# Kernel tuning notes

Hardware: AMD Instinct MI355X
Metric: run time of the kernel (lower is better)

The kernel has to match this reference:

```python
import jax, jax.numpy as jnp
import numpy as np

D_MODEL = 1024
D_FF = 2048
N_EXPERTS = 8
Z_LOSS_COEF = 0.001


def setup_inputs() -> dict:
    key = jax.random.key(0)
    kx, kr, k1, k3, k2 = jax.random.split(key, 5)
    s_in = 1.0 / np.sqrt(D_MODEL)
    s_ff = 1.0 / np.sqrt(D_FF)
    return {
        "x": jax.random.normal(kx, (4, 2048, D_MODEL), dtype=jnp.float32),
        # router: nn.Linear(d_model, num_experts, bias=False) -> weight [E, D]
        "Wr": jax.random.normal(kr, (N_EXPERTS, D_MODEL), dtype=jnp.float32) * s_in,
        # stacked expert weights, torch Linear layout [out, in]
        "W1": jax.random.normal(k1, (N_EXPERTS, D_FF, D_MODEL), dtype=jnp.float32) * s_in,
        "W3": jax.random.normal(k3, (N_EXPERTS, D_FF, D_MODEL), dtype=jnp.float32) * s_in,
        "W2": jax.random.normal(k2, (N_EXPERTS, D_MODEL, D_FF), dtype=jnp.float32) * s_ff,
    }


def reference(x, Wr, W1, W3, W2):
    B, S, D = x.shape
    E = Wr.shape[0]
    xf = x.reshape(B * S, D)          # [T, D]
    T = xf.shape[0]

    # --- router ---
    logits = xf @ Wr.T                # [T, E]
    probs = jax.nn.softmax(logits, axis=-1)
    top2_p, top2_i = jax.lax.top_k(probs, 2)          # [T, 2]
    top2_p = top2_p / (jnp.sum(top2_p, axis=-1, keepdims=True) + 1e-9)

    # dense gate matrix: zero for unselected experts (same math as index_add combine)
    gates = jnp.zeros((T, E), jnp.float32).at[jnp.arange(T)[:, None], top2_i].add(top2_p)

    # --- experts (SwiGLU), computed per-expert over all tokens, masked by gates ---
    h1 = jax.nn.silu(jnp.einsum('td,efd->etf', xf, W1))   # [E, T, F]
    h3 = jnp.einsum('td,efd->etf', xf, W3)                 # [E, T, F]
    y = jnp.einsum('etf,edf->etd', h1 * h3, W2)            # [E, T, D]
    out = jnp.einsum('etd,te->td', y.astype(jnp.float32), gates)
    out = out.astype(x.dtype).reshape(B, S, D)

    # --- losses ---
    z = jax.nn.logsumexp(logits.astype(jnp.float32), axis=-1)
    router_loss = Z_LOSS_COEF * jnp.mean(z * z)

    importance = jnp.sum(probs.astype(jnp.float32), axis=0) / T   # [E]
    top1 = top2_i[:, 0]
    load = jnp.zeros((E,), jnp.float32).at[top1].add(1.0) / T
    aux_loss = jnp.sum(importance * load) * E

    return out, router_loss, aux_loss
```

## Files before the change

kernel.cpp:

```cpp
#include <hip/hip_runtime.h>
#include <stdint.h>

#define NT 8192
#define DM 1024
#define DF 2048
#define RT_BLOCKS 256

typedef __attribute__((ext_vector_type(8))) short short8;
typedef __attribute__((ext_vector_type(4))) float f32x4;

__device__ __forceinline__ unsigned short f2bf(float f) {
  uint32_t x = __float_as_uint(f);
  return (unsigned short)((x + 0x7fffu + ((x >> 16) & 1u)) >> 16);
}

__device__ __forceinline__ void gload16(const void* g, void* l) {
  __builtin_amdgcn_global_load_lds(
      (const __attribute__((address_space(1))) uint32_t*)g,
      (__attribute__((address_space(3))) uint32_t*)l, 16, 0, 0);
}

__global__ void k_cvtw(const float4* __restrict__ w1, const float4* __restrict__ w3,
                       const float4* __restrict__ w2,
                       ushort4* __restrict__ w13, ushort4* __restrict__ w2bf) {
  int s = blockIdx.y;
  const float4* src = (s == 0) ? w1 : (s == 1) ? w3 : w2;
  int n4 = 8 * DF * DM / 4;
  int i = blockIdx.x * blockDim.x + threadIdx.x;
  int st = gridDim.x * blockDim.x;
  for (; i < n4; i += st) {
    float4 v = src[i];
    ushort4 o;
    o.x = f2bf(v.x); o.y = f2bf(v.y); o.z = f2bf(v.z); o.w = f2bf(v.w);
    if (s == 2) {
      w2bf[i] = o;
    } else {
      int e = i >> 19;
      int rem = i & ((1 << 19) - 1);
      int f = rem >> 8;
      int k4 = rem & 255;
      w13[((size_t)e << 20) + (size_t)(2 * f + s) * 256 + k4] = o;
    }
  }
}

__global__ void k_router(const float* __restrict__ x, const float* __restrict__ wr,
                         int* cntb, int* cnt1, float* imp, float* z2,
                         int* epack, float2* gts, unsigned short* __restrict__ xbf) {
  int lane = threadIdx.x & 63;
  int wid = threadIdx.x >> 6;
  const float4* w4 = (const float4*)wr;

  float imp_acc[8] = {0.f, 0.f, 0.f, 0.f, 0.f, 0.f, 0.f, 0.f};
  float z2_acc = 0.f;
  int cb_acc[8] = {0, 0, 0, 0, 0, 0, 0, 0};
  int c1_acc[8] = {0, 0, 0, 0, 0, 0, 0, 0};

  for (int t = blockIdx.x * 4 + wid; t < NT; t += RT_BLOCKS * 4) {
    const float4* x4 = (const float4*)(x + (size_t)t * DM);
    ushort4* xb4 = (ushort4*)(xbf + (size_t)t * DM);
    float4 xv[4];
    #pragma unroll
    for (int j = 0; j < 4; ++j) {
      xv[j] = x4[lane + 64 * j];
      ushort4 o;
      o.x = f2bf(xv[j].x); o.y = f2bf(xv[j].y); o.z = f2bf(xv[j].z); o.w = f2bf(xv[j].w);
      xb4[lane + 64 * j] = o;
    }
    float p[8];
    #pragma unroll
    for (int e = 0; e < 8; ++e) p[e] = 0.f;
    #pragma unroll
    for (int j = 0; j < 4; ++j) {
      #pragma unroll
      for (int e = 0; e < 8; ++e) {
        float4 wv = w4[e * 256 + lane + 64 * j];
        p[e] += xv[j].x * wv.x + xv[j].y * wv.y + xv[j].z * wv.z + xv[j].w * wv.w;
      }
    }
    #pragma unroll
    for (int off = 32; off > 0; off >>= 1) {
      #pragma unroll
      for (int e = 0; e < 8; ++e) p[e] += __shfl_down(p[e], off);
    }
    if (lane == 0) {
      float m = p[0];
      #pragma unroll
      for (int e = 1; e < 8; ++e) m = fmaxf(m, p[e]);
      float pr[8], s = 0.f;
      #pragma unroll
      for (int e = 0; e < 8; ++e) { pr[e] = expf(p[e] - m); s += pr[e]; }
      float inv = 1.f / s;
      #pragma unroll
      for (int e = 0; e < 8; ++e) pr[e] *= inv;
      float z = m + logf(s);
      int e0 = 0; float b0 = p[0];
      #pragma unroll
      for (int e = 1; e < 8; ++e) { if (p[e] > b0) { b0 = p[e]; e0 = e; } }
      int e1 = -1; float b1 = -1e30f;
      #pragma unroll
      for (int e = 0; e < 8; ++e) { if (e != e0 && p[e] > b1) { b1 = p[e]; e1 = e; } }
      float p0 = 0.f, p1 = 0.f;
      #pragma unroll
      for (int e = 0; e < 8; ++e) {
        p0 = (e == e0) ? pr[e] : p0;
        p1 = (e == e1) ? pr[e] : p1;
      }
      float gs = p0 + p1 + 1e-9f;
      epack[t] = e0 | (e1 << 16);
      gts[t] = make_float2(p0 / gs, p1 / gs);
      z2_acc += z * z;
      #pragma unroll
      for (int e = 0; e < 8; ++e) {
        imp_acc[e] += pr[e];
        cb_acc[e] += (e == e0) + (e == e1);
        c1_acc[e] += (e == e0);
      }
    }
  }

  __shared__ float simp[4][8];
  __shared__ float sz2[4];
  __shared__ int scb[4][8];
  __shared__ int sc1[4][8];
  if (lane == 0) {
    #pragma unroll
    for (int e = 0; e < 8; ++e) { simp[wid][e] = imp_acc[e]; scb[wid][e] = cb_acc[e]; sc1[wid][e] = c1_acc[e]; }
    sz2[wid] = z2_acc;
  }
  __syncthreads();
  int tid = threadIdx.x;
  if (tid < 8) {
    float s = simp[0][tid] + simp[1][tid] + simp[2][tid] + simp[3][tid];
    int b = scb[0][tid] + scb[1][tid] + scb[2][tid] + scb[3][tid];
    int o = sc1[0][tid] + sc1[1][tid] + sc1[2][tid] + sc1[3][tid];
    atomicAdd(&imp[tid], s);
    atomicAdd(&cntb[tid], b);
    atomicAdd(&cnt1[tid], o);
  } else if (tid == 8) {
    atomicAdd(z2, sz2[0] + sz2[1] + sz2[2] + sz2[3]);
  }
}

__global__ void k_finalize(const int* cntb, const int* cnt1, const float* imp,
                           const float* z2, int* offs, float* otail) {
  if (threadIdx.x == 0 && blockIdx.x == 0) {
    int o = 0;
    for (int e = 0; e < 8; ++e) { offs[e] = o; o += cntb[e]; }
    otail[0] = 1e-3f * z2[0] / (float)NT;
    float aux = 0.f;
    for (int e = 0; e < 8; ++e)
      aux += (imp[e] / (float)NT) * ((float)cnt1[e] / (float)NT);
    otail[1] = aux * 8.f;
  }
}

__global__ void k_scatter(const int* __restrict__ epack, const float2* __restrict__ gts,
                          const int* __restrict__ offs,
                          int* __restrict__ btok, int* __restrict__ pos) {
  int e = blockIdx.x;
  int lane = threadIdx.x;
  int base = offs[e];
  int run = 0;
  for (int j0 = 0; j0 < 2 * NT; j0 += 64) {
    int j = j0 + lane;
    int t = j >> 1;
    int ep = epack[t];
    int sel = (j & 1) ? (ep >> 16) : (ep & 0xffff);
    bool f = (sel == e);
    unsigned long long m = __ballot(f);
    int rank = __popcll(m & ((1ull << lane) - 1ull));
    if (f) {
      int slot = base + run + rank;
      btok[slot] = t;
      pos[j] = slot;
    }
    run += __popcll(m);
  }
}

__global__ __launch_bounds__(512, 2) void k_ffn1(
    const unsigned short* __restrict__ xb,
    const unsigned short* __restrict__ w13,
    const int* __restrict__ offs, const int* __restrict__ cnts,
    const int* __restrict__ btok,
    unsigned short* __restrict__ hg) {
  int e = blockIdx.z;
  int cnt = cnts[e];
  int m0 = blockIdx.y * 256;
  if (m0 >= cnt) return;
  int n0 = blockIdx.x * 256;
  int off = offs[e];
  __shared__ __align__(16) short As[2][256 * 64];
  __shared__ __align__(16) short Bs[2][256 * 64];
  __shared__ int tok[256];
  int tid = threadIdx.x, lane = tid & 63, wid = tid >> 6;
  if (tid < 256) {
    int r = m0 + tid; if (r > cnt - 1) r = cnt - 1;
    tok[tid] = btok[off + r];
  }
  __syncthreads();

  int rin = lane >> 3;
  int scol = (((lane & 7) ^ rin)) * 8;
  const unsigned short* w13e = w13 + ((size_t)e << 22);
  const unsigned short* asrc[4];
  const unsigned short* bsrc[4];
  int dofs[4];
  #pragma unroll
  for (int i = 0; i < 4; ++i) {
    int ch = wid * 4 + i;
    int rr = ch * 8 + rin;
    asrc[i] = xb + (size_t)tok[rr] * DM + scol;
    bsrc[i] = w13e + (size_t)(n0 + rr) * DM + scol;
    dofs[i] = ch * 512;
  }

  int wm = wid >> 2, wn = wid & 3;
  int g = lane >> 4;
  int l7 = lane & 7;
  int fr = lane & 15;
  f32x4 acc[8][4] = {};

  #pragma unroll
  for (int i = 0; i < 4; ++i) {
    gload16(asrc[i], &As[0][dofs[i]]);
    gload16(bsrc[i], &Bs[0][dofs[i]]);
  }
  __syncthreads();

  int cur = 0;
  const int NK = DM / 64;
  for (int kt = 0; kt < NK; ++kt) {
    if (kt + 1 < NK) {
      int k0 = (kt + 1) * 64;
      #pragma unroll
      for (int i = 0; i < 4; ++i) {
        gload16(asrc[i] + k0, &As[cur ^ 1][dofs[i]]);
        gload16(bsrc[i] + k0, &Bs[cur ^ 1][dofs[i]]);
      }
    }
    #pragma unroll
    for (int kk = 0; kk < 2; ++kk) {
      int G = kk * 4 + g;
      short8 a[8], b[4];
      #pragma unroll
      for (int mi = 0; mi < 8; ++mi) {
        int r = wm * 128 + mi * 16 + fr;
        a[mi] = *(const short8*)&As[cur][r * 64 + ((G ^ l7) * 8)];
      }
      #pragma unroll
      for (int ni = 0; ni < 4; ++ni) {
        int r = wn * 64 + ni * 16 + fr;
        b[ni] = *(const short8*)&Bs[cur][r * 64 + ((G ^ l7) * 8)];
      }
      #pragma unroll
      for (int mi = 0; mi < 8; ++mi) {
        #pragma unroll
        for (int ni = 0; ni < 4; ++ni)
          acc[mi][ni] = __builtin_amdgcn_mfma_f32_16x16x32_bf16(a[mi], b[ni], acc[mi][ni], 0, 0, 0);
      }
    }
    __syncthreads();
    cur ^= 1;
  }

  int c = lane & 15, r4 = (lane >> 4) * 4;
  bool evenc = ((c & 1) == 0);
  #pragma unroll
  for (int mi = 0; mi < 8; ++mi) {
    #pragma unroll
    for (int rg = 0; rg < 4; ++rg) {
      int gr = m0 + wm * 128 + mi * 16 + r4 + rg;
      #pragma unroll
      for (int ni = 0; ni < 4; ++ni) {
        float a1 = acc[mi][ni][rg];
        float a3 = __shfl_xor(a1, 1);
        if (evenc && gr < cnt) {
          int f = (n0 + wn * 64 + ni * 16 + c) >> 1;
          float h = (a1 / (1.f + __expf(-a1))) * a3;
          hg[(size_t)(off + gr) * DF + f] = f2bf(h);
        }
      }
    }
  }
}

__global__ __launch_bounds__(512, 2) void k_ffn2(
    const unsigned short* __restrict__ hg,
    const unsigned short* __restrict__ w2b,
    const int* __restrict__ offs, const int* __restrict__ cnts,
    float* __restrict__ ys) {
  int e = blockIdx.z;
  int cnt = cnts[e];
  int m0 = blockIdx.y * 256;
  if (m0 >= cnt) return;
  int n0 = blockIdx.x * 256;
  int off = offs[e];
  __shared__ __align__(16) short As[2][256 * 64];
  __shared__ __align__(16) short Bs[2][256 * 64];
  int tid = threadIdx.x, lane = tid & 63, wid = tid >> 6;

  int rin = lane >> 3;
  int scol = (((lane & 7) ^ rin)) * 8;
  const unsigned short* w2e = w2b + ((size_t)e << 21);
  const unsigned short* asrc[4];
  const unsigned short* bsrc[4];
  int dofs[4];
  #pragma unroll
  for (int i = 0; i < 4; ++i) {
    int ch = wid * 4 + i;
    int rr = ch * 8 + rin;
    int ar = m0 + rr; if (ar > cnt - 1) ar = cnt - 1;
    asrc[i] = hg + (size_t)(off + ar) * DF + scol;
    bsrc[i] = w2e + (size_t)(n0 + rr) * DF + scol;
    dofs[i] = ch * 512;
  }

  int wm = wid >> 2, wn = wid & 3;
  int g = lane >> 4;
  int l7 = lane & 7;
  int fr = lane & 15;
  f32x4 acc[8][4] = {};

  #pragma unroll
  for (int i = 0; i < 4; ++i) {
    gload16(asrc[i], &As[0][dofs[i]]);
    gload16(bsrc[i], &Bs[0][dofs[i]]);
  }
  __syncthreads();

  int cur = 0;
  const int NK = DF / 64;
  for (int kt = 0; kt < NK; ++kt) {
    if (kt + 1 < NK) {
      int k0 = (kt + 1) * 64;
      #pragma unroll
      for (int i = 0; i < 4; ++i) {
        gload16(asrc[i] + k0, &As[cur ^ 1][dofs[i]]);
        gload16(bsrc[i] + k0, &Bs[cur ^ 1][dofs[i]]);
      }
    }
    #pragma unroll
    for (int kk = 0; kk < 2; ++kk) {
      int G = kk * 4 + g;
      short8 a[8], b[4];
      #pragma unroll
      for (int mi = 0; mi < 8; ++mi) {
        int r = wm * 128 + mi * 16 + fr;
        a[mi] = *(const short8*)&As[cur][r * 64 + ((G ^ l7) * 8)];
      }
      #pragma unroll
      for (int ni = 0; ni < 4; ++ni) {
        int r = wn * 64 + ni * 16 + fr;
        b[ni] = *(const short8*)&Bs[cur][r * 64 + ((G ^ l7) * 8)];
      }
      #pragma unroll
      for (int mi = 0; mi < 8; ++mi) {
        #pragma unroll
        for (int ni = 0; ni < 4; ++ni)
          acc[mi][ni] = __builtin_amdgcn_mfma_f32_16x16x32_bf16(a[mi], b[ni], acc[mi][ni], 0, 0, 0);
      }
    }
    __syncthreads();
    cur ^= 1;
  }

  int c = lane & 15, r4 = (lane >> 4) * 4;
  #pragma unroll
  for (int mi = 0; mi < 8; ++mi) {
    #pragma unroll
    for (int rg = 0; rg < 4; ++rg) {
      int gr = m0 + wm * 128 + mi * 16 + r4 + rg;
      if (gr < cnt) {
        float* yrow = ys + (size_t)(off + gr) * DM + n0;
        #pragma unroll
        for (int ni = 0; ni < 4; ++ni)
          yrow[wn * 64 + ni * 16 + c] = acc[mi][ni][rg];
      }
    }
  }
}

__global__ void k_gather(const float* __restrict__ ys, const int* __restrict__ pos,
                         const float2* __restrict__ gts, float* __restrict__ out) {
  int idx = blockIdx.x * blockDim.x + threadIdx.x;
  int t = idx >> 8;
  int d4 = idx & 255;
  float2 g = gts[t];
  const float4* y0 = (const float4*)(ys + (size_t)pos[2 * t] * DM) + d4;
  const float4* y1 = (const float4*)(ys + (size_t)pos[2 * t + 1] * DM) + d4;
  float4 a = *y0, b = *y1, o;
  o.x = g.x * a.x + g.y * b.x;
  o.y = g.x * a.y + g.y * b.y;
  o.z = g.x * a.z + g.y * b.z;
  o.w = g.x * a.w + g.y * b.w;
  ((float4*)out)[idx] = o;
}


extern "C" void kernel_launch(void* const* d_in, const int* in_sizes, int n_in,
                              void* d_out, int out_size, void* d_ws, size_t ws_size,
                              hipStream_t stream) {
  const float* x  = (const float*)d_in[0];
  const float* wr = (const float*)d_in[1];
  const float* w1 = (const float*)d_in[2];
  const float* w3 = (const float*)d_in[3];
  const float* w2 = (const float*)d_in[4];
  float* out = (float*)d_out;

  uint8_t* ws = (uint8_t*)d_ws;
  int*    cntb   = (int*)(ws + 0);
  int*    cnt1   = (int*)(ws + 32);
  int*    offs   = (int*)(ws + 96);
  float*  imp    = (float*)(ws + 128);
  float*  z2     = (float*)(ws + 160);
  int*    epack  = (int*)(ws + 4096);
  float2* gts    = (float2*)(ws + 36864);
  int*    btok   = (int*)(ws + 102400);
  int*    pos    = (int*)(ws + 167936);
  unsigned short* xbf  = (unsigned short*)(ws + 233472);
  unsigned short* w13  = (unsigned short*)(ws + 17010688);
  unsigned short* w2bf = (unsigned short*)(ws + 84119552);
  unsigned short* hg   = (unsigned short*)(ws + 117673984);
  float*          ysb  = (float*)(ws + 17010688);

  hipMemsetAsync(ws, 0, 4096, stream);

  k_cvtw<<<dim3(2048, 3), 256, 0, stream>>>(
      (const float4*)w1, (const float4*)w3, (const float4*)w2,
      (ushort4*)w13, (ushort4*)w2bf);

  k_router<<<RT_BLOCKS, 256, 0, stream>>>(x, wr, cntb, cnt1, imp, z2, epack, gts, xbf);
  k_finalize<<<1, 64, 0, stream>>>(cntb, cnt1, imp, z2, offs, out + (size_t)NT * DM);
  k_scatter<<<8, 64, 0, stream>>>(epack, gts, offs, btok, pos);

  k_ffn1<<<dim3(16, 64, 8), 512, 0, stream>>>(xbf, w13, offs, cntb, btok, hg);
  k_ffn2<<<dim3(4, 64, 8), 512, 0, stream>>>(hg, w2bf, offs, cntb, ysb);
  k_gather<<<NT * DM / 4 / 256, 256, 0, stream>>>(ysb, pos, gts, out);
}
```

Baseline: 562.3 us.

## Pipeline FFN GEMMs with a 4-slot LDS ring and interleaved load/MFMA phases

Both expert GEMM kernels move from a double-buffered 64-wide K loop to a 4-slot ring of 32-wide K slices. Each slice is gated by an explicit vmcnt wait and a raw barrier. Global-to-LDS loads for the next slices are issued between the two halves of the MFMA work, which raises wave priority with s_setprio. The LDS tile layout is also changed to pack row pairs into 64-element rows with a new XOR swizzle. The goal is better overlap of memory and matrix work and fewer bank conflicts, at the cost of hand-managed wait counts that could break correctness if miscounted.

```diff
diff --git a/kernel.cpp b/kernel.cpp
--- a/kernel.cpp
+++ b/kernel.cpp
@@ -8,10 +8,11 @@
 
 typedef __attribute__((ext_vector_type(8))) short short8;
 typedef __attribute__((ext_vector_type(4))) float f32x4;
-
-__device__ __forceinline__ unsigned short f2bf(float f) {
+typedef unsigned short us;
+
+__device__ __forceinline__ us f2bf(float f) {
   uint32_t x = __float_as_uint(f);
-  return (unsigned short)((x + 0x7fffu + ((x >> 16) & 1u)) >> 16);
+  return (us)((x + 0x7fffu + ((x >> 16) & 1u)) >> 16);
 }
 
 __device__ __forceinline__ void gload16(const void* g, void* l) {
@@ -46,7 +47,7 @@
 
 __global__ void k_router(const float* __restrict__ x, const float* __restrict__ wr,
                          int* cntb, int* cnt1, float* imp, float* z2,
-                         int* epack, float2* gts, unsigned short* __restrict__ xbf) {
+                         int* epack, float2* gts, us* __restrict__ xbf) {
   int lane = threadIdx.x & 63;
   int wid = threadIdx.x >> 6;
   const float4* w4 = (const float4*)wr;
@@ -179,20 +180,41 @@
   }
 }
 
+
+#define FFN_PHASE_READS(slot, mi0, a, b, DOB)                                   \
+  if (DOB) {                                                                    \
+    _Pragma("unroll")                                                           \
+    for (int ni = 0; ni < 4; ++ni)                                              \
+      b[ni] = *(const short8*)&Bs[slot][boff + ni * 512];                       \
+  }                                                                             \
+  _Pragma("unroll")                                                             \
+  for (int mi = 0; mi < 4; ++mi)                                                \
+    a[mi] = *(const short8*)&As[slot][aoff + (mi0 + mi) * 512];
+
+#define FFN_PHASE_MFMA(mi0, a, b)                                               \
+  __builtin_amdgcn_s_setprio(1);                                                \
+  _Pragma("unroll")                                                             \
+  for (int mi = 0; mi < 4; ++mi) {                                              \
+    _Pragma("unroll")                                                           \
+    for (int ni = 0; ni < 4; ++ni)                                              \
+      acc[mi0 + mi][ni] =                                                       \
+          __builtin_amdgcn_mfma_f32_16x16x32_bf16(a[mi], b[ni],                 \
+                                                  acc[mi0 + mi][ni], 0, 0, 0);  \
+  }                                                                             \
+  __builtin_amdgcn_s_setprio(0);
+
 __global__ __launch_bounds__(512, 2) void k_ffn1(
-    const unsigned short* __restrict__ xb,
-    const unsigned short* __restrict__ w13,
+    const us* __restrict__ xb, const us* __restrict__ w13,
     const int* __restrict__ offs, const int* __restrict__ cnts,
-    const int* __restrict__ btok,
-    unsigned short* __restrict__ hg) {
+    const int* __restrict__ btok, us* __restrict__ hg) {
   int e = blockIdx.z;
   int cnt = cnts[e];
   int m0 = blockIdx.y * 256;
   if (m0 >= cnt) return;
   int n0 = blockIdx.x * 256;
   int off = offs[e];
-  __shared__ __align__(16) short As[2][256 * 64];
-  __shared__ __align__(16) short Bs[2][256 * 64];
+  __shared__ __align__(16) short As[4][8192];
+  __shared__ __align__(16) short Bs[4][8192];
   __shared__ int tok[256];
   int tid = threadIdx.x, lane = tid & 63, wid = tid >> 6;
   if (tid < 256) {
@@ -201,69 +223,62 @@
   }
   __syncthreads();
 
-  int rin = lane >> 3;
-  int scol = (((lane & 7) ^ rin)) * 8;
-  const unsigned short* w13e = w13 + ((size_t)e << 22);
-  const unsigned short* asrc[4];
-  const unsigned short* bsrc[4];
-  int dofs[4];
-  #pragma unroll
-  for (int i = 0; i < 4; ++i) {
-    int ch = wid * 4 + i;
-    int rr = ch * 8 + rin;
-    asrc[i] = xb + (size_t)tok[rr] * DM + scol;
-    bsrc[i] = w13e + (size_t)(n0 + rr) * DM + scol;
-    dofs[i] = ch * 512;
-  }
+  int posun = (lane & 7) ^ ((lane >> 3) & 7);
+  int rl0 = wid * 32 + ((lane >> 3) << 1) + (posun >> 2);
+  int rl1 = rl0 + 16;
+  int gcol = (posun & 3) * 8;
+  const us* w13e = w13 + ((size_t)e << 22);
+  const us* a0 = xb + (size_t)tok[rl0] * DM + gcol;
+  const us* a1 = xb + (size_t)tok[rl1] * DM + gcol;
+  const us* b0 = w13e + (size_t)(n0 + rl0) * DM + gcol;
+  const us* b1 = w13e + (size_t)(n0 + rl1) * DM + gcol;
+  int dst0 = wid * 1024, dst1 = wid * 1024 + 512;
+
+  auto stageA = [&](int ko, int slot) {
+    gload16(a0 + ko, &As[slot][dst0]);
+    gload16(a1 + ko, &As[slot][dst1]);
+  };
+  auto stageB = [&](int ko, int slot) {
+    gload16(b0 + ko, &Bs[slot][dst0]);
+    gload16(b1 + ko, &Bs[slot][dst1]);
+  };
 
   int wm = wid >> 2, wn = wid & 3;
-  int g = lane >> 4;
-  int l7 = lane & 7;
-  int fr = lane & 15;
+  int fr = lane & 15, glog = lane >> 4;
+  int pos = (((fr & 1) << 2) | glog) ^ ((fr >> 1) & 7);
+  int aoff = (wm * 64 + (fr >> 1)) * 64 + pos * 8;
+  int boff = (wn * 32 + (fr >> 1)) * 64 + pos * 8;
   f32x4 acc[8][4] = {};
 
-  #pragma unroll
-  for (int i = 0; i < 4; ++i) {
-    gload16(asrc[i], &As[0][dofs[i]]);
-    gload16(bsrc[i], &Bs[0][dofs[i]]);
-  }
-  __syncthreads();
-
-  int cur = 0;
+  stageA(0, 0); stageB(0, 0); stageA(32, 1); stageB(32, 1);
+
   const int NK = DM / 64;
-  for (int kt = 0; kt < NK; ++kt) {
-    if (kt + 1 < NK) {
-      int k0 = (kt + 1) * 64;
-      #pragma unroll
-      for (int i = 0; i < 4; ++i) {
-        gload16(asrc[i] + k0, &As[cur ^ 1][dofs[i]]);
-        gload16(bsrc[i] + k0, &Bs[cur ^ 1][dofs[i]]);
-      }
-    }
-    #pragma unroll
-    for (int kk = 0; kk < 2; ++kk) {
-      int G = kk * 4 + g;
-      short8 a[8], b[4];
-      #pragma unroll
-      for (int mi = 0; mi < 8; ++mi) {
-        int r = wm * 128 + mi * 16 + fr;
-        a[mi] = *(const short8*)&As[cur][r * 64 + ((G ^ l7) * 8)];
-      }
-      #pragma unroll
-      for (int ni = 0; ni < 4; ++ni) {
-        int r = wn * 64 + ni * 16 + fr;
-        b[ni] = *(const short8*)&Bs[cur][r * 64 + ((G ^ l7) * 8)];
-      }
-      #pragma unroll
-      for (int mi = 0; mi < 8; ++mi) {
-        #pragma unroll
-        for (int ni = 0; ni < 4; ++ni)
-          acc[mi][ni] = __builtin_amdgcn_mfma_f32_16x16x32_bf16(a[mi], b[ni], acc[mi][ni], 0, 0, 0);
-      }
-    }
-    __syncthreads();
-    cur ^= 1;
-  }
+  for (int t = 0; t < NK; ++t) {
+    int sl0 = (2 * t) & 3, sl1 = sl0 ^ 1;
+    int kn = (t + 1 < NK) ? (t + 1) : t;
+    int sn0 = (sl0 + 2) & 3, sn1 = sn0 ^ 1;
+    int kb = kn * 64;
+    short8 a[4], b[4];
+
+    asm volatile("s_waitcnt vmcnt(4)" ::: "memory");
+    __builtin_amdgcn_s_barrier();
+    FFN_PHASE_READS(sl0, 0, a, b, 1)
+    stageA(kb, sn0);
+    FFN_PHASE_MFMA(0, a, b)
+    FFN_PHASE_READS(sl0, 4, a, b, 0)
+    stageB(kb, sn0);
+    FFN_PHASE_MFMA(4, a, b)
+
+    asm volatile("s_waitcnt vmcnt(4)" ::: "memory");
+    __builtin_amdgcn_s_barrier();
+    FFN_PHASE_READS(sl1, 0, a, b, 1)
+    stageA(kb + 32, sn1);
+    FFN_PHASE_MFMA(0, a, b)
+    FFN_PHASE_READS(sl1, 4, a, b, 0)
+    stageB(kb + 32, sn1);
+    FFN_PHASE_MFMA(4, a, b)
+  }
+  asm volatile("s_waitcnt vmcnt(0)" ::: "memory");
 
   int c = lane & 15, r4 = (lane >> 4) * 4;
   bool evenc = ((c & 1) == 0);
@@ -274,11 +289,11 @@
       int gr = m0 + wm * 128 + mi * 16 + r4 + rg;
       #pragma unroll
       for (int ni = 0; ni < 4; ++ni) {
-        float a1 = acc[mi][ni][rg];
-        float a3 = __shfl_xor(a1, 1);
+        float a1v = acc[mi][ni][rg];
+        float a3v = __shfl_xor(a1v, 1);
         if (evenc && gr < cnt) {
           int f = (n0 + wn * 64 + ni * 16 + c) >> 1;
-          float h = (a1 / (1.f + __expf(-a1))) * a3;
+          float h = (a1v / (1.f + __expf(-a1v))) * a3v;
           hg[(size_t)(off + gr) * DF + f] = f2bf(h);
         }
       }
@@ -287,8 +302,7 @@
 }
 
 __global__ __launch_bounds__(512, 2) void k_ffn2(
-    const unsigned short* __restrict__ hg,
-    const unsigned short* __restrict__ w2b,
+    const us* __restrict__ hg, const us* __restrict__ w2b,
     const int* __restrict__ offs, const int* __restrict__ cnts,
     float* __restrict__ ys) {
   int e = blockIdx.z;
@@ -297,74 +311,68 @@
   if (m0 >= cnt) return;
   int n0 = blockIdx.x * 256;
   int off = offs[e];
-  __shared__ __align__(16) short As[2][256 * 64];
-  __shared__ __align__(16) short Bs[2][256 * 64];
+  __shared__ __align__(16) short As[4][8192];
+  __shared__ __align__(16) short Bs[4][8192];
   int tid = threadIdx.x, lane = tid & 63, wid = tid >> 6;
 
-  int rin = lane >> 3;
-  int scol = (((lane & 7) ^ rin)) * 8;
-  const unsigned short* w2e = w2b + ((size_t)e << 21);
-  const unsigned short* asrc[4];
-  const unsigned short* bsrc[4];
-  int dofs[4];
-  #pragma unroll
-  for (int i = 0; i < 4; ++i) {
-    int ch = wid * 4 + i;
-    int rr = ch * 8 + rin;
-    int ar = m0 + rr; if (ar > cnt - 1) ar = cnt - 1;
-    asrc[i] = hg + (size_t)(off + ar) * DF + scol;
-    bsrc[i] = w2e + (size_t)(n0 + rr) * DF + scol;
-    dofs[i] = ch * 512;
-  }
+  int posun = (lane & 7) ^ ((lane >> 3) & 7);
+  int rl0 = wid * 32 + ((lane >> 3) << 1) + (posun >> 2);
+  int rl1 = rl0 + 16;
+  int gcol = (posun & 3) * 8;
+  int ar0 = m0 + rl0; if (ar0 > cnt - 1) ar0 = cnt - 1;
+  int ar1 = m0 + rl1; if (ar1 > cnt - 1) ar1 = cnt - 1;
+  const us* w2e = w2b + ((size_t)e << 21);
+  const us* a0 = hg + (size_t)(off + ar0) * DF + gcol;
+  const us* a1 = hg + (size_t)(off + ar1) * DF + gcol;
+  const us* b0 = w2e + (size_t)(n0 + rl0) * DF + gcol;
+  const us* b1 = w2e + (size_t)(n0 + rl1) * DF + gcol;
+  int dst0 = wid * 1024, dst1 = wid * 1024 + 512;
+
+  auto stageA = [&](int ko, int slot) {
+    gload16(a0 + ko, &As[slot][dst0]);
+    gload16(a1 + ko, &As[slot][dst1]);
+  };
+  auto stageB = [&](int ko, int slot) {
+    gload16(b0 + ko, &Bs[slot][dst0]);
+    gload16(b1 + ko, &Bs[slot][dst1]);
+  };
 
   int wm = wid >> 2, wn = wid & 3;
-  int g = lane >> 4;
-  int l7 = lane & 7;
-  int fr = lane & 15;
+  int fr = lane & 15, glog = lane >> 4;
+  int pos = (((fr & 1) << 2) | glog) ^ ((fr >> 1) & 7);
+  int aoff = (wm * 64 + (fr >> 1)) * 64 + pos * 8;
+  int boff = (wn * 32 + (fr >> 1)) * 64 + pos * 8;
   f32x4 acc[8][4] = {};
 
-  #pragma unroll
-  for (int i = 0; i < 4; ++i) {
-    gload16(asrc[i], &As[0][dofs[i]]);
-    gload16(bsrc[i], &Bs[0][dofs[i]]);
-  }
-  __syncthreads();
-
-  int cur = 0;
+  stageA(0, 0); stageB(0, 0); stageA(32, 1); stageB(32, 1);
+
   const int NK = DF / 64;
-  for (int kt = 0; kt < NK; ++kt) {
-    if (kt + 1 < NK) {
-      int k0 = (kt + 1) * 64;
-      #pragma unroll
-      for (int i = 0; i < 4; ++i) {
-        gload16(asrc[i] + k0, &As[cur ^ 1][dofs[i]]);
-        gload16(bsrc[i] + k0, &Bs[cur ^ 1][dofs[i]]);
-      }
-    }
-    #pragma unroll
-    for (int kk = 0; kk < 2; ++kk) {
-      int G = kk * 4 + g;
-      short8 a[8], b[4];
-      #pragma unroll
-      for (int mi = 0; mi < 8; ++mi) {
-        int r = wm * 128 + mi * 16 + fr;
-        a[mi] = *(const short8*)&As[cur][r * 64 + ((G ^ l7) * 8)];
-      }
-      #pragma unroll
-      for (int ni = 0; ni < 4; ++ni) {
-        int r = wn * 64 + ni * 16 + fr;
-        b[ni] = *(const short8*)&Bs[cur][r * 64 + ((G ^ l7) * 8)];
-      }
-      #pragma unroll
-      for (int mi = 0; mi < 8; ++mi) {
-        #pragma unroll
-        for (int ni = 0; ni < 4; ++ni)
-          acc[mi][ni] = __builtin_amdgcn_mfma_f32_16x16x32_bf16(a[mi], b[ni], acc[mi][ni], 0, 0, 0);
-      }
-    }
-    __syncthreads();
-    cur ^= 1;
-  }
+  for (int t = 0; t < NK; ++t) {
+    int sl0 = (2 * t) & 3, sl1 = sl0 ^ 1;
+    int kn = (t + 1 < NK) ? (t + 1) : t;
+    int sn0 = (sl0 + 2) & 3, sn1 = sn0 ^ 1;
+    int kb = kn * 64;
+    short8 a[4], b[4];
+
+    asm volatile("s_waitcnt vmcnt(4)" ::: "memory");
+    __builtin_amdgcn_s_barrier();
+    FFN_PHASE_READS(sl0, 0, a, b, 1)
+    stageA(kb, sn0);
+    FFN_PHASE_MFMA(0, a, b)
+    FFN_PHASE_READS(sl0, 4, a, b, 0)
+    stageB(kb, sn0);
+    FFN_PHASE_MFMA(4, a, b)
+
+    asm volatile("s_waitcnt vmcnt(4)" ::: "memory");
+    __builtin_amdgcn_s_barrier();
+    FFN_PHASE_READS(sl1, 0, a, b, 1)
+    stageA(kb + 32, sn1);
+    FFN_PHASE_MFMA(0, a, b)
+    FFN_PHASE_READS(sl1, 4, a, b, 0)
+    stageB(kb + 32, sn1);
+    FFN_PHASE_MFMA(4, a, b)
+  }
+  asm volatile("s_waitcnt vmcnt(0)" ::: "memory");
 
   int c = lane & 15, r4 = (lane >> 4) * 4;
   #pragma unroll
@@ -419,11 +427,11 @@
   float2* gts    = (float2*)(ws + 36864);
   int*    btok   = (int*)(ws + 102400);
   int*    pos    = (int*)(ws + 167936);
-  unsigned short* xbf  = (unsigned short*)(ws + 233472);
-  unsigned short* w13  = (unsigned short*)(ws + 17010688);
-  unsigned short* w2bf = (unsigned short*)(ws + 84119552);
-  unsigned short* hg   = (unsigned short*)(ws + 117673984);
-  float*          ysb  = (float*)(ws + 17010688);
+  us*     xbf    = (us*)(ws + 233472);
+  us*     w13    = (us*)(ws + 17010688);
+  us*     w2bf   = (us*)(ws + 84119552);
+  us*     hg     = (us*)(ws + 117673984);
+  float*  ysb    = (float*)(ws + 17010688);
 
   hipMemsetAsync(ws, 0, 4096, stream);
 
```

After: 549.3 us. 1.02x faster.

## Halve FFN GEMM LDS footprint with k-split swizzled layout, drop double buffering

Applied to the files above, without the earlier changes.

Both expert GEMM kernels now keep a single k-step in LDS, stored as two 32-column halves with a new XOR swizzle. This replaces the 256x64 double-buffered tiles, so each block uses half as much LDS. The software prefetch is gone, so each step loads, syncs, computes and syncs again. The aim is to fit two blocks per CU and let them hide each other's load latency instead of prefetching within one block. The min-blocks hint is dropped from launch bounds, which gives the compiler more register freedom, but a block now stalls on global loads if the other block cannot cover for it.

```diff
diff --git a/kernel.cpp b/kernel.cpp
--- a/kernel.cpp
+++ b/kernel.cpp
@@ -8,10 +8,11 @@
 
 typedef __attribute__((ext_vector_type(8))) short short8;
 typedef __attribute__((ext_vector_type(4))) float f32x4;
-
-__device__ __forceinline__ unsigned short f2bf(float f) {
+typedef unsigned short us;
+
+__device__ __forceinline__ us f2bf(float f) {
   uint32_t x = __float_as_uint(f);
-  return (unsigned short)((x + 0x7fffu + ((x >> 16) & 1u)) >> 16);
+  return (us)((x + 0x7fffu + ((x >> 16) & 1u)) >> 16);
 }
 
 __device__ __forceinline__ void gload16(const void* g, void* l) {
@@ -46,7 +47,7 @@
 
 __global__ void k_router(const float* __restrict__ x, const float* __restrict__ wr,
                          int* cntb, int* cnt1, float* imp, float* z2,
-                         int* epack, float2* gts, unsigned short* __restrict__ xbf) {
+                         int* epack, float2* gts, us* __restrict__ xbf) {
   int lane = threadIdx.x & 63;
   int wid = threadIdx.x >> 6;
   const float4* w4 = (const float4*)wr;
@@ -179,20 +180,19 @@
   }
 }
 
-__global__ __launch_bounds__(512, 2) void k_ffn1(
-    const unsigned short* __restrict__ xb,
-    const unsigned short* __restrict__ w13,
+
+__global__ __launch_bounds__(512) void k_ffn1(
+    const us* __restrict__ xb, const us* __restrict__ w13,
     const int* __restrict__ offs, const int* __restrict__ cnts,
-    const int* __restrict__ btok,
-    unsigned short* __restrict__ hg) {
+    const int* __restrict__ btok, us* __restrict__ hg) {
   int e = blockIdx.z;
   int cnt = cnts[e];
   int m0 = blockIdx.y * 256;
   if (m0 >= cnt) return;
   int n0 = blockIdx.x * 256;
   int off = offs[e];
-  __shared__ __align__(16) short As[2][256 * 64];
-  __shared__ __align__(16) short Bs[2][256 * 64];
+  __shared__ __align__(16) short As[2][8192];
+  __shared__ __align__(16) short Bs[2][8192];
   __shared__ int tok[256];
   int tid = threadIdx.x, lane = tid & 63, wid = tid >> 6;
   if (tid < 256) {
@@ -201,59 +201,44 @@
   }
   __syncthreads();
 
-  int rin = lane >> 3;
-  int scol = (((lane & 7) ^ rin)) * 8;
-  const unsigned short* w13e = w13 + ((size_t)e << 22);
-  const unsigned short* asrc[4];
-  const unsigned short* bsrc[4];
-  int dofs[4];
-  #pragma unroll
-  for (int i = 0; i < 4; ++i) {
-    int ch = wid * 4 + i;
-    int rr = ch * 8 + rin;
-    asrc[i] = xb + (size_t)tok[rr] * DM + scol;
-    bsrc[i] = w13e + (size_t)(n0 + rr) * DM + scol;
-    dofs[i] = ch * 512;
-  }
+  int posun = (lane & 7) ^ ((lane >> 3) & 7);
+  int rbase = wid * 16 + ((lane >> 3) << 1) + (posun >> 2);
+  int gcol = (posun & 3) * 8;
+  const us* w13e = w13 + ((size_t)e << 22);
+  const us* aP0 = xb + (size_t)tok[rbase] * DM + gcol;
+  const us* aP1 = xb + (size_t)tok[rbase + 128] * DM + gcol;
+  const us* bP0 = w13e + (size_t)(n0 + rbase) * DM + gcol;
+  const us* bP1 = w13e + (size_t)(n0 + rbase + 128) * DM + gcol;
+  int dst0 = wid * 512, dst1 = 4096 + wid * 512;
 
   int wm = wid >> 2, wn = wid & 3;
-  int g = lane >> 4;
-  int l7 = lane & 7;
-  int fr = lane & 15;
+  int fr = lane & 15, glog = lane >> 4;
+  int pos = (((fr & 1) << 2) | glog) ^ ((fr >> 1) & 7);
+  int aoff = (wm * 64 + (fr >> 1)) * 64 + pos * 8;
+  int boff = (wn * 32 + (fr >> 1)) * 64 + pos * 8;
   f32x4 acc[8][4] = {};
 
-  #pragma unroll
-  for (int i = 0; i < 4; ++i) {
-    gload16(asrc[i], &As[0][dofs[i]]);
-    gload16(bsrc[i], &Bs[0][dofs[i]]);
-  }
-  __syncthreads();
-
-  int cur = 0;
   const int NK = DM / 64;
   for (int kt = 0; kt < NK; ++kt) {
-    if (kt + 1 < NK) {
-      int k0 = (kt + 1) * 64;
-      #pragma unroll
-      for (int i = 0; i < 4; ++i) {
-        gload16(asrc[i] + k0, &As[cur ^ 1][dofs[i]]);
-        gload16(bsrc[i] + k0, &Bs[cur ^ 1][dofs[i]]);
-      }
-    }
+    int k0 = kt * 64;
+    #pragma unroll
+    for (int h = 0; h < 2; ++h) {
+      int ko = k0 + h * 32;
+      gload16(aP0 + ko, &As[h][dst0]);
+      gload16(aP1 + ko, &As[h][dst1]);
+      gload16(bP0 + ko, &Bs[h][dst0]);
+      gload16(bP1 + ko, &Bs[h][dst1]);
+    }
+    __syncthreads();
     #pragma unroll
     for (int kk = 0; kk < 2; ++kk) {
-      int G = kk * 4 + g;
       short8 a[8], b[4];
       #pragma unroll
-      for (int mi = 0; mi < 8; ++mi) {
-        int r = wm * 128 + mi * 16 + fr;
-        a[mi] = *(const short8*)&As[cur][r * 64 + ((G ^ l7) * 8)];
-      }
-      #pragma unroll
-      for (int ni = 0; ni < 4; ++ni) {
-        int r = wn * 64 + ni * 16 + fr;
-        b[ni] = *(const short8*)&Bs[cur][r * 64 + ((G ^ l7) * 8)];
-      }
+      for (int mi = 0; mi < 8; ++mi)
+        a[mi] = *(const short8*)&As[kk][aoff + mi * 512];
+      #pragma unroll
+      for (int ni = 0; ni < 4; ++ni)
+        b[ni] = *(const short8*)&Bs[kk][boff + ni * 512];
       #pragma unroll
       for (int mi = 0; mi < 8; ++mi) {
         #pragma unroll
@@ -262,7 +247,6 @@
       }
     }
     __syncthreads();
-    cur ^= 1;
   }
 
   int c = lane & 15, r4 = (lane >> 4) * 4;
@@ -274,11 +258,11 @@
       int gr = m0 + wm * 128 + mi * 16 + r4 + rg;
       #pragma unroll
       for (int ni = 0; ni < 4; ++ni) {
-        float a1 = acc[mi][ni][rg];
-        float a3 = __shfl_xor(a1, 1);
+        float a1v = acc[mi][ni][rg];
+        float a3v = __shfl_xor(a1v, 1);
         if (evenc && gr < cnt) {
           int f = (n0 + wn * 64 + ni * 16 + c) >> 1;
-          float h = (a1 / (1.f + __expf(-a1))) * a3;
+          float h = (a1v / (1.f + __expf(-a1v))) * a3v;
           hg[(size_t)(off + gr) * DF + f] = f2bf(h);
         }
       }
@@ -286,9 +270,8 @@
   }
 }
 
-__global__ __launch_bounds__(512, 2) void k_ffn2(
-    const unsigned short* __restrict__ hg,
-    const unsigned short* __restrict__ w2b,
+__global__ __launch_bounds__(512) void k_ffn2(
+    const us* __restrict__ hg, const us* __restrict__ w2b,
     const int* __restrict__ offs, const int* __restrict__ cnts,
     float* __restrict__ ys) {
   int e = blockIdx.z;
@@ -297,64 +280,50 @@
   if (m0 >= cnt) return;
   int n0 = blockIdx.x * 256;
   int off = offs[e];
-  __shared__ __align__(16) short As[2][256 * 64];
-  __shared__ __align__(16) short Bs[2][256 * 64];
+  __shared__ __align__(16) short As[2][8192];
+  __shared__ __align__(16) short Bs[2][8192];
   int tid = threadIdx.x, lane = tid & 63, wid = tid >> 6;
 
-  int rin = lane >> 3;
-  int scol = (((lane & 7) ^ rin)) * 8;
-  const unsigned short* w2e = w2b + ((size_t)e << 21);
-  const unsigned short* asrc[4];
-  const unsigned short* bsrc[4];
-  int dofs[4];
-  #pragma unroll
-  for (int i = 0; i < 4; ++i) {
-    int ch = wid * 4 + i;
-    int rr = ch * 8 + rin;
-    int ar = m0 + rr; if (ar > cnt - 1) ar = cnt - 1;
-    asrc[i] = hg + (size_t)(off + ar) * DF + scol;
-    bsrc[i] = w2e + (size_t)(n0 + rr) * DF + scol;
-    dofs[i] = ch * 512;
-  }
+  int posun = (lane & 7) ^ ((lane >> 3) & 7);
+  int rbase = wid * 16 + ((lane >> 3) << 1) + (posun >> 2);
+  int gcol = (posun & 3) * 8;
+  int ar0 = m0 + rbase;       if (ar0 > cnt - 1) ar0 = cnt - 1;
+  int ar1 = m0 + rbase + 128; if (ar1 > cnt - 1) ar1 = cnt - 1;
+  const us* w2e = w2b + ((size_t)e << 21);
+  const us* aP0 = hg + (size_t)(off + ar0) * DF + gcol;
+  const us* aP1 = hg + (size_t)(off + ar1) * DF + gcol;
+  const us* bP0 = w2e + (size_t)(n0 + rbase) * DF + gcol;
+  const us* bP1 = w2e + (size_t)(n0 + rbase + 128) * DF + gcol;
+  int dst0 = wid * 512, dst1 = 4096 + wid * 512;
 
   int wm = wid >> 2, wn = wid & 3;
-  int g = lane >> 4;
-  int l7 = lane & 7;
-  int fr = lane & 15;
+  int fr = lane & 15, glog = lane >> 4;
+  int pos = (((fr & 1) << 2) | glog) ^ ((fr >> 1) & 7);
+  int aoff = (wm * 64 + (fr >> 1)) * 64 + pos * 8;
+  int boff = (wn * 32 + (fr >> 1)) * 64 + pos * 8;
   f32x4 acc[8][4] = {};
 
-  #pragma unroll
-  for (int i = 0; i < 4; ++i) {
-    gload16(asrc[i], &As[0][dofs[i]]);
-    gload16(bsrc[i], &Bs[0][dofs[i]]);
-  }
-  __syncthreads();
-
-  int cur = 0;
   const int NK = DF / 64;
   for (int kt = 0; kt < NK; ++kt) {
-    if (kt + 1 < NK) {
-      int k0 = (kt + 1) * 64;
-      #pragma unroll
-      for (int i = 0; i < 4; ++i) {
-        gload16(asrc[i] + k0, &As[cur ^ 1][dofs[i]]);
-        gload16(bsrc[i] + k0, &Bs[cur ^ 1][dofs[i]]);
-      }
-    }
+    int k0 = kt * 64;
+    #pragma unroll
+    for (int h = 0; h < 2; ++h) {
+      int ko = k0 + h * 32;
+      gload16(aP0 + ko, &As[h][dst0]);
+      gload16(aP1 + ko, &As[h][dst1]);
+      gload16(bP0 + ko, &Bs[h][dst0]);
+      gload16(bP1 + ko, &Bs[h][dst1]);
+    }
+    __syncthreads();
     #pragma unroll
     for (int kk = 0; kk < 2; ++kk) {
-      int G = kk * 4 + g;
       short8 a[8], b[4];
       #pragma unroll
-      for (int mi = 0; mi < 8; ++mi) {
-        int r = wm * 128 + mi * 16 + fr;
-        a[mi] = *(const short8*)&As[cur][r * 64 + ((G ^ l7) * 8)];
-      }
-      #pragma unroll
-      for (int ni = 0; ni < 4; ++ni) {
-        int r = wn * 64 + ni * 16 + fr;
-        b[ni] = *(const short8*)&Bs[cur][r * 64 + ((G ^ l7) * 8)];
-      }
+      for (int mi = 0; mi < 8; ++mi)
+        a[mi] = *(const short8*)&As[kk][aoff + mi * 512];
+      #pragma unroll
+      for (int ni = 0; ni < 4; ++ni)
+        b[ni] = *(const short8*)&Bs[kk][boff + ni * 512];
       #pragma unroll
       for (int mi = 0; mi < 8; ++mi) {
         #pragma unroll
@@ -363,7 +332,6 @@
       }
     }
     __syncthreads();
-    cur ^= 1;
   }
 
   int c = lane & 15, r4 = (lane >> 4) * 4;
@@ -419,11 +387,11 @@
   float2* gts    = (float2*)(ws + 36864);
   int*    btok   = (int*)(ws + 102400);
   int*    pos    = (int*)(ws + 167936);
-  unsigned short* xbf  = (unsigned short*)(ws + 233472);
-  unsigned short* w13  = (unsigned short*)(ws + 17010688);
-  unsigned short* w2bf = (unsigned short*)(ws + 84119552);
-  unsigned short* hg   = (unsigned short*)(ws + 117673984);
-  float*          ysb  = (float*)(ws + 17010688);
+  us*     xbf    = (us*)(ws + 233472);
+  us*     w13    = (us*)(ws + 17010688);
+  us*     w2bf   = (us*)(ws + 84119552);
+  us*     hg     = (us*)(ws + 117673984);
+  float*  ysb    = (float*)(ws + 17010688);
 
   hipMemsetAsync(ws, 0, 4096, stream);
 
```

New measurement: 617.5 us. 9.8% more time.
